# Performance work log

Hardware: AMD Instinct MI355X
Metric: run time of the kernel (lower is better)

The kernel has to match this reference:

```python
import jax, jax.numpy as jnp
import numpy as np

N_NODES = 100000
NUM_GRAPHS = 128
NEG_SLOPE = 0.2


def gat_layer(x, ei, W, a_src, a_dst, b, heads, ch, concat):
    """PyG-style GATConv (v1) with self-loops already included in ei.
    ei[0]=source j, ei[1]=target i; softmax over incoming edges of each target."""
    N = x.shape[0]
    h = (x @ W).reshape(N, heads, ch)                      # [N,H,C]
    asrc = jnp.sum(h * a_src, axis=-1)                     # [N,H]
    adst = jnp.sum(h * a_dst, axis=-1)                     # [N,H]
    src, dst = ei[0], ei[1]
    e = jax.nn.leaky_relu(asrc[src] + adst[dst], NEG_SLOPE)  # [E,H]
    m = jax.ops.segment_max(e, dst, num_segments=N)        # stable softmax per target
    ex = jnp.exp(e - m[dst])
    denom = jax.ops.segment_sum(ex, dst, num_segments=N)
    alpha = ex / denom[dst]                                # [E,H]
    msg = h[src] * alpha[:, :, None]                       # [E,H,C] gather+weight
    out = jax.ops.segment_sum(msg, dst, num_segments=N)    # scatter-add aggregate
    out = out.reshape(N, heads * ch) if concat else out.mean(axis=1)
    return out + b


def setup_inputs() -> dict:
    key = jax.random.key(0)
    ks = jax.random.split(key, 16)
    d_in = 128
    x = jax.random.normal(ks[0], (N_NODES, d_in), dtype=jnp.float32)
    edge_index = jax.random.randint(ks[1], (2, 1600000), 0, N_NODES, dtype=jnp.int64)
    batch = jnp.sort(jax.random.randint(ks[2], (N_NODES,), 0, NUM_GRAPHS, dtype=jnp.int64))
    s = lambda k, shp, fan: jax.random.normal(k, shp, dtype=jnp.float32) / np.sqrt(fan)
    params = dict(
        W1=s(ks[3], (d_in, 4 * 48), d_in),
        a_src1=0.1 * jax.random.normal(ks[4], (4, 48), dtype=jnp.float32),
        a_dst1=0.1 * jax.random.normal(ks[5], (4, 48), dtype=jnp.float32),
        b1=jnp.zeros((4 * 48,), dtype=jnp.float32),
        W2=s(ks[6], (192, 96), 192),
        a_src2=0.1 * jax.random.normal(ks[7], (1, 96), dtype=jnp.float32),
        a_dst2=0.1 * jax.random.normal(ks[8], (1, 96), dtype=jnp.float32),
        b2=jnp.zeros((96,), dtype=jnp.float32),
        fc1_w=s(ks[9], (96, 192), 96),
        fc1_b=jnp.zeros((192,), dtype=jnp.float32),
        fc2_w=s(ks[10], (192, 96), 192),
        fc2_b=jnp.zeros((96,), dtype=jnp.float32),
    )
    return dict(x=x, edge_index=edge_index, batch=batch, **params)


def reference(x, edge_index, batch, W1, a_src1, a_dst1, b1, W2, a_src2, a_dst2, b2,
              fc1_w, fc1_b, fc2_w, fc2_b):
    N = x.shape[0]
    loops = jnp.arange(N, dtype=edge_index.dtype)
    ei = jnp.concatenate([edge_index, jnp.stack([loops, loops])], axis=1)
    h = jax.nn.relu(gat_layer(x, ei, W1, a_src1, a_dst1, b1, heads=4, ch=48, concat=True))
    h = jax.nn.relu(gat_layer(h, ei, W2, a_src2, a_dst2, b2, heads=1, ch=96, concat=True))
    # global mean pool over graphs
    sums = jax.ops.segment_sum(h, batch, num_segments=NUM_GRAPHS)          # [G,96]
    counts = jax.ops.segment_sum(jnp.ones((N,), h.dtype), batch, num_segments=NUM_GRAPHS)
    pooled = sums / jnp.maximum(counts, 1.0)[:, None]
    z = jax.nn.relu(pooled @ fc1_w + fc1_b)
    return z @ fc2_w + fc2_b
```

## Files before the change

### kernel.cpp

```cpp
#include <hip/hip_runtime.h>


#define LRELU(x) fmaxf((x), 0.2f * (x))

using bf16x8 = __attribute__((ext_vector_type(8))) short;
using f32x16 = __attribute__((ext_vector_type(16))) float;

#define NSB 256

__device__ inline unsigned short f2bf(float f) {
  unsigned u = __builtin_bit_cast(unsigned, f);
  return (unsigned short)((u + 0x7fffu + ((u >> 16) & 1u)) >> 16);
}
__device__ inline float bf2f(unsigned short h) {
  return __builtin_bit_cast(float, (unsigned)h << 16);
}
__device__ inline float bfLO(unsigned v) { return __builtin_bit_cast(float, v << 16); }
__device__ inline float bfHI(unsigned v) { return __builtin_bit_cast(float, v & 0xffff0000u); }
__device__ inline unsigned packbf(float a, float b) {
  return (unsigned)f2bf(a) | ((unsigned)f2bf(b) << 16);
}

__device__ inline void wave_lds_fence() {
  __builtin_amdgcn_wave_barrier();
  __builtin_amdgcn_s_waitcnt(0xc07f);
  __builtin_amdgcn_wave_barrier();
}


__global__ __launch_bounds__(256) void k_hist2(const int* __restrict__ dst, int E, int chunk,
                                               int NBK, int* __restrict__ cntmat) {
  __shared__ int lh[512];
  int b = blockIdx.x, t = threadIdx.x;
  for (int i = t; i < NBK; i += 256) lh[i] = 0;
  __syncthreads();
  int beg = b * chunk, end = min(E, beg + chunk);
  for (int e = beg + t; e < end; e += 256) atomicAdd(&lh[dst[e] >> 8], 1);
  __syncthreads();
  for (int i = t; i < NBK; i += 256) cntmat[i * NSB + b] = lh[i];
}

__global__ __launch_bounds__(256) void k_rowscan(int* __restrict__ cntmat,
                                                 int* __restrict__ bucket_tot) {
  int k = blockIdx.x, t = threadIdx.x;
  __shared__ int sc[256];
  int v = cntmat[k * NSB + t];
  sc[t] = v;
  __syncthreads();
  for (int off = 1; off < 256; off <<= 1) {
    int add = (t >= off) ? sc[t - off] : 0;
    __syncthreads();
    sc[t] += add;
    __syncthreads();
  }
  cntmat[k * NSB + t] = sc[t] - v;
  if (t == 255) bucket_tot[k] = sc[t];
}

__global__ __launch_bounds__(512) void k_bscan(const int* __restrict__ bucket_tot, int NBK,
                                               int* __restrict__ bucket_off,
                                               int* __restrict__ row_off, int N, int E) {
  __shared__ int sc[512];
  int t = threadIdx.x;
  int v = (t < NBK) ? bucket_tot[t] : 0;
  sc[t] = v;
  __syncthreads();
  for (int off = 1; off < 512; off <<= 1) {
    int add = (t >= off) ? sc[t - off] : 0;
    __syncthreads();
    sc[t] += add;
    __syncthreads();
  }
  int excl = sc[t] - v;
  if (t < NBK) {
    bucket_off[t] = excl;
    if (t == NBK - 1) bucket_off[NBK] = excl + v;
  }
  if (t == 0) row_off[N] = E + N;
}

__global__ __launch_bounds__(256) void k_scatter2(const int* __restrict__ src,
                                                  const int* __restrict__ dst, int E, int chunk,
                                                  int NBK, const int* __restrict__ bucket_off,
                                                  const int* __restrict__ cntmat,
                                                  int* __restrict__ pairs) {
  __shared__ int base[512];
  __shared__ int cur[512];
  int b = blockIdx.x, t = threadIdx.x;
  for (int i = t; i < NBK; i += 256) {
    base[i] = bucket_off[i] + cntmat[i * NSB + b];
    cur[i] = 0;
  }
  __syncthreads();
  int beg = b * chunk, end = min(E, beg + chunk);
  for (int e = beg + t; e < end; e += 256) {
    int s = src[e], d = dst[e];
    int k = d >> 8;
    int loc = atomicAdd(&cur[k], 1);
    pairs[base[k] + loc] = (s << 8) | (d & 255);
  }
}

#define BBUILD_CAP 8448
__global__ __launch_bounds__(256) void k_bbuild(const int* __restrict__ pairs,
                                                const int* __restrict__ bucket_off,
                                                int N, int* __restrict__ row_off,
                                                int* __restrict__ col) {
  int b = blockIdx.x;
  int t = threadIdx.x;
  int base_d = b * 256;
  int nd = N - base_d;
  if (nd > 256) nd = 256;
  int pbeg = bucket_off[b], pend = bucket_off[b + 1];
  int cntb = pend - pbeg;
  int colbase = pbeg + base_d;

  __shared__ int hist[256];
  __shared__ int scn[256];
  __shared__ int cur[256];
  __shared__ int colL[BBUILD_CAP];
  hist[t] = 0;
  __syncthreads();
  for (int p = pbeg + t; p < pend; p += 256) atomicAdd(&hist[pairs[p] & 255], 1);
  __syncthreads();
  int v = (t < nd) ? hist[t] + 1 : 0;
  scn[t] = v;
  __syncthreads();
  for (int off = 1; off < 256; off <<= 1) {
    int add = (t >= off) ? scn[t - off] : 0;
    __syncthreads();
    scn[t] += add;
    __syncthreads();
  }
  int excl = scn[t] - v;
  if (t < nd) row_off[base_d + t] = colbase + excl;
  int total = cntb + nd;
  if (total <= BBUILD_CAP) {
    cur[t] = excl;
    if (t < nd) colL[excl + hist[t]] = base_d + t;
    __syncthreads();
    for (int p = pbeg + t; p < pend; p += 256) {
      int w = pairs[p];
      int lp = atomicAdd(&cur[w & 255], 1);
      colL[lp] = w >> 8;
    }
    __syncthreads();
    for (int i = t; i < total; i += 256) col[colbase + i] = colL[i];
  } else {
    cur[t] = excl;
    if (t < nd) col[colbase + excl + hist[t]] = base_d + t;
    __syncthreads();
    for (int p = pbeg + t; p < pend; p += 256) {
      int w = pairs[p];
      int lp = atomicAdd(&cur[w & 255], 1);
      col[colbase + lp] = w >> 8;
    }
  }
}


__global__ __launch_bounds__(256) void k_convW(const float* __restrict__ W1,
                                               const float* __restrict__ W2,
                                               unsigned short* __restrict__ T1h,
                                               unsigned short* __restrict__ T1l,
                                               unsigned short* __restrict__ T2h,
                                               unsigned short* __restrict__ T2l) {
  const int E1 = 128 * 192;
  const int E2 = 192 * 96;
  int idx = blockIdx.x * 256 + threadIdx.x;
  if (idx < E1) {
    int k = idx / 192, n = idx - k * 192;
    float w = W1[idx];
    unsigned short hi = f2bf(w);
    unsigned short lo = f2bf(w - bf2f(hi));
    T1h[n * 128 + k] = hi;
    T1l[n * 128 + k] = lo;
  } else if (idx < E1 + E2) {
    int i2 = idx - E1;
    int k = i2 / 96, n = i2 - k * 96;
    float w = W2[i2];
    unsigned short hi = f2bf(w);
    unsigned short lo = f2bf(w - bf2f(hi));
    T2h[n * 192 + k] = hi;
    T2l[n * 192 + k] = lo;
  }
}


template <int K, int N, bool A_BF16>
__global__ __launch_bounds__(256) void k_gemm_mfma(const void* __restrict__ Ap,
                                                   const unsigned short* __restrict__ Bh,
                                                   const unsigned short* __restrict__ Bl,
                                                   unsigned short* __restrict__ C, int M) {
  constexpr int NT = N / 32;
  __shared__ unsigned short As[128 * 40];
  __shared__ unsigned short Bhs[N * 40];
  __shared__ unsigned short Bls[N * 40];
  int tid = threadIdx.x;
  int wave = tid >> 6, lane = tid & 63;
  int bm = blockIdx.x * 128;

  f32x16 acc[NT];
#pragma unroll
  for (int t = 0; t < NT; ++t)
#pragma unroll
    for (int i = 0; i < 16; ++i) acc[t][i] = 0.f;

  for (int k0 = 0; k0 < K; k0 += 32) {
#pragma unroll
    for (int i = 0; i < 2; ++i) {
      int unit = tid + i * 256;
      int r = unit >> 2, u = unit & 3;
      int gr = bm + r;
      uint4 o = make_uint4(0, 0, 0, 0);
      if (gr < M) {
        if (A_BF16) {
          o = *(const uint4*)((const unsigned short*)Ap + (size_t)gr * K + k0 + u * 8);
        } else {
          const float* af = (const float*)Ap + (size_t)gr * K + k0 + u * 8;
          float4 v0 = *(const float4*)af;
          float4 v1 = *(const float4*)(af + 4);
          o.x = (unsigned)f2bf(v0.x) | ((unsigned)f2bf(v0.y) << 16);
          o.y = (unsigned)f2bf(v0.z) | ((unsigned)f2bf(v0.w) << 16);
          o.z = (unsigned)f2bf(v1.x) | ((unsigned)f2bf(v1.y) << 16);
          o.w = (unsigned)f2bf(v1.z) | ((unsigned)f2bf(v1.w) << 16);
        }
      }
      *(uint4*)&As[r * 40 + u * 8] = o;
    }
    for (int unit = tid; unit < N * 4; unit += 256) {
      int n = unit >> 2, u = unit & 3;
      *(uint4*)&Bhs[n * 40 + u * 8] = *(const uint4*)&Bh[n * K + k0 + u * 8];
      *(uint4*)&Bls[n * 40 + u * 8] = *(const uint4*)&Bl[n * K + k0 + u * 8];
    }
    __syncthreads();

    int arow = wave * 32 + (lane & 31);
    int fo = (lane >> 5) * 8;
#pragma unroll
    for (int s = 0; s < 2; ++s) {
      bf16x8 af = *(const bf16x8*)&As[arow * 40 + s * 16 + fo];
#pragma unroll
      for (int t = 0; t < NT; ++t) {
        bf16x8 bh = *(const bf16x8*)&Bhs[(t * 32 + (lane & 31)) * 40 + s * 16 + fo];
        bf16x8 bl = *(const bf16x8*)&Bls[(t * 32 + (lane & 31)) * 40 + s * 16 + fo];
        acc[t] = __builtin_amdgcn_mfma_f32_32x32x16_bf16(af, bh, acc[t], 0, 0, 0);
        acc[t] = __builtin_amdgcn_mfma_f32_32x32x16_bf16(af, bl, acc[t], 0, 0, 0);
      }
    }
    __syncthreads();
  }

#pragma unroll
  for (int t = 0; t < NT; ++t) {
    int col = t * 32 + (lane & 31);
#pragma unroll
    for (int r = 0; r < 16; ++r) {
      int row = wave * 32 + (r & 3) + 8 * (r >> 2) + 4 * (lane >> 5);
      int gr = bm + row;
      if (gr < M) C[(size_t)gr * N + col] = f2bf(acc[t][r]);
    }
  }
}


__global__ __launch_bounds__(256) void k_coef1(const unsigned short* __restrict__ h,
                                               const float* __restrict__ a_src,
                                               const float* __restrict__ a_dst,
                                               float* __restrict__ asrc,
                                               float* __restrict__ adst, int N) {
  int node = blockIdx.x * 4 + (threadIdx.x >> 6);
  if (node >= N) return;
  int m = threadIdx.x & 63;
  const unsigned* hp = (const unsigned*)h + (size_t)node * 96;
  unsigned va = hp[m];
  float x0 = bfLO(va), x1 = bfHI(va);
  float2 as = *(const float2*)&a_src[2 * m];
  float2 ad = *(const float2*)&a_dst[2 * m];
  float pas = x0 * as.x + x1 * as.y;
  float pad = x0 * ad.x + x1 * ad.y;
  int ha = m / 24;
  float pbs = 0.f, pbd = 0.f;
  int hb = (m < 8) ? 2 : 3;
  if (m < 32) {
    unsigned vb = hp[64 + m];
    float y0 = bfLO(vb), y1 = bfHI(vb);
    float2 bs = *(const float2*)&a_src[128 + 2 * m];
    float2 bd = *(const float2*)&a_dst[128 + 2 * m];
    pbs = y0 * bs.x + y1 * bs.y;
    pbd = y0 * bd.x + y1 * bd.y;
  }
  float4 cs, cd;
  cs.x = (ha == 0) ? pas : 0.f;
  cs.y = (ha == 1) ? pas : 0.f;
  cs.z = ((ha == 2) ? pas : 0.f) + ((hb == 2) ? pbs : 0.f);
  cs.w = (hb == 3) ? pbs : 0.f;
  cd.x = (ha == 0) ? pad : 0.f;
  cd.y = (ha == 1) ? pad : 0.f;
  cd.z = ((ha == 2) ? pad : 0.f) + ((hb == 2) ? pbd : 0.f);
  cd.w = (hb == 3) ? pbd : 0.f;
#pragma unroll
  for (int off = 1; off < 64; off <<= 1) {
    cs.x += __shfl_xor(cs.x, off);
    cs.y += __shfl_xor(cs.y, off);
    cs.z += __shfl_xor(cs.z, off);
    cs.w += __shfl_xor(cs.w, off);
    cd.x += __shfl_xor(cd.x, off);
    cd.y += __shfl_xor(cd.y, off);
    cd.z += __shfl_xor(cd.z, off);
    cd.w += __shfl_xor(cd.w, off);
  }
  if (m == 0) {
    *(float4*)&asrc[node * 4] = cs;
    *(float4*)&adst[node * 4] = cd;
  }
}

__global__ __launch_bounds__(256) void k_coef2(const unsigned short* __restrict__ h,
                                               const float* __restrict__ a_src,
                                               const float* __restrict__ a_dst,
                                               float* __restrict__ asrc,
                                               float* __restrict__ adst, int N) {
  int node = blockIdx.x * 4 + (threadIdx.x >> 6);
  if (node >= N) return;
  int m = threadIdx.x & 63;
  float ps = 0.f, pd = 0.f;
  if (m < 48) {
    unsigned v = ((const unsigned*)h)[(size_t)node * 48 + m];
    float x0 = bfLO(v), x1 = bfHI(v);
    float2 as = *(const float2*)&a_src[2 * m];
    float2 ad = *(const float2*)&a_dst[2 * m];
    ps = x0 * as.x + x1 * as.y;
    pd = x0 * ad.x + x1 * ad.y;
  }
#pragma unroll
  for (int off = 1; off < 64; off <<= 1) {
    ps += __shfl_xor(ps, off);
    pd += __shfl_xor(pd, off);
  }
  if (m == 0) {
    asrc[node] = ps;
    adst[node] = pd;
  }
}


__global__ __launch_bounds__(256) void k_agg1(const unsigned short* __restrict__ h,
                                              const float* __restrict__ asrc,
                                              const float* __restrict__ adst,
                                              const int* __restrict__ row_off,
                                              const int* __restrict__ col,
                                              const float* __restrict__ b1,
                                              unsigned short* __restrict__ out, int N) {
  __shared__ int sL[4][64];
  __shared__ float wL[4][64][4];
  int wid = threadIdx.x >> 6;
  int node = blockIdx.x * 4 + wid;
  if (node >= N) return;
  int lane = threadIdx.x & 63;
  int q = lane >> 4;
  int m = lane & 15;
  int hA = m / 6;
  int hB = (m < 4) ? 2 : 3;
  int beg = __builtin_amdgcn_readfirstlane(row_off[node]);
  int end = __builtin_amdgcn_readfirstlane(row_off[node + 1]);
  float4 ad = *(const float4*)&adst[node * 4];
  float accA0 = 0, accA1 = 0, accA2 = 0, accA3 = 0;
  float accA4 = 0, accA5 = 0, accA6 = 0, accA7 = 0;
  float accB0 = 0, accB1 = 0, accB2 = 0, accB3 = 0;
  float da = 0.f, db = 0.f;
  const unsigned* h32 = (const unsigned*)h;
  for (int base = beg; base < end; base += 64) {
    int cnt = end - base;
    if (cnt > 64) cnt = 64;
    int s = 0;
    float w0 = 0.f, w1 = 0.f, w2 = 0.f, w3 = 0.f;
    if (lane < cnt) {
      s = col[base + lane];
      float4 as = *(const float4*)&asrc[s * 4];
      w0 = __expf(LRELU(as.x + ad.x));
      w1 = __expf(LRELU(as.y + ad.y));
      w2 = __expf(LRELU(as.z + ad.z));
      w3 = __expf(LRELU(as.w + ad.w));
    }
    sL[wid][lane] = s;
    *(float4*)&wL[wid][lane][0] = make_float4(w0, w1, w2, w3);
    wave_lds_fence();
    int jmax = (cnt + 3) & ~3;
#pragma unroll 4
    for (int j = 0; j < jmax; j += 4) {
      int je = j + q;
      int sj = sL[wid][je];
      float wa = wL[wid][je][hA];
      float wb = wL[wid][je][hB];
      const unsigned* hp = h32 + (size_t)sj * 96;
      uint4 va = *(const uint4*)(hp + 4 * m);
      uint2 vb = *(const uint2*)(hp + 64 + 2 * m);
      da += wa;
      db += wb;
      accA0 += wa * bfLO(va.x);
      accA1 += wa * bfHI(va.x);
      accA2 += wa * bfLO(va.y);
      accA3 += wa * bfHI(va.y);
      accA4 += wa * bfLO(va.z);
      accA5 += wa * bfHI(va.z);
      accA6 += wa * bfLO(va.w);
      accA7 += wa * bfHI(va.w);
      accB0 += wb * bfLO(vb.x);
      accB1 += wb * bfHI(vb.x);
      accB2 += wb * bfLO(vb.y);
      accB3 += wb * bfHI(vb.y);
    }
    __builtin_amdgcn_wave_barrier();
  }
#define RED2(x) x += __shfl_xor(x, 16); x += __shfl_xor(x, 32)
  RED2(da); RED2(db);
  RED2(accA0); RED2(accA1); RED2(accA2); RED2(accA3);
  RED2(accA4); RED2(accA5); RED2(accA6); RED2(accA7);
  RED2(accB0); RED2(accB1); RED2(accB2); RED2(accB3);
#undef RED2
  if (q == 0) {
    float ra = 1.f / da, rb = 1.f / db;
    float4 biA0 = *(const float4*)&b1[8 * m];
    float4 biA1 = *(const float4*)&b1[8 * m + 4];
    float4 biB = *(const float4*)&b1[128 + 4 * m];
    unsigned* op = (unsigned*)(out + (size_t)node * 192);
    uint4 pa;
    pa.x = packbf(fmaxf(accA0 * ra + biA0.x, 0.f), fmaxf(accA1 * ra + biA0.y, 0.f));
    pa.y = packbf(fmaxf(accA2 * ra + biA0.z, 0.f), fmaxf(accA3 * ra + biA0.w, 0.f));
    pa.z = packbf(fmaxf(accA4 * ra + biA1.x, 0.f), fmaxf(accA5 * ra + biA1.y, 0.f));
    pa.w = packbf(fmaxf(accA6 * ra + biA1.z, 0.f), fmaxf(accA7 * ra + biA1.w, 0.f));
    *(uint4*)(op + 4 * m) = pa;
    uint2 pb;
    pb.x = packbf(fmaxf(accB0 * rb + biB.x, 0.f), fmaxf(accB1 * rb + biB.y, 0.f));
    pb.y = packbf(fmaxf(accB2 * rb + biB.z, 0.f), fmaxf(accB3 * rb + biB.w, 0.f));
    *(uint2*)(op + 64 + 2 * m) = pb;
  }
}

__global__ __launch_bounds__(256) void k_agg2(const unsigned short* __restrict__ h,
                                              const float* __restrict__ asrc,
                                              const float* __restrict__ adst,
                                              const int* __restrict__ row_off,
                                              const int* __restrict__ col,
                                              const float* __restrict__ b2,
                                              float* __restrict__ out, int N) {
  __shared__ int2 eL[4][64];
  int wid = threadIdx.x >> 6;
  int node = blockIdx.x * 4 + wid;
  if (node >= N) return;
  int lane = threadIdx.x & 63;
  int g = lane >> 4;
  int m = lane & 15;
  int beg = __builtin_amdgcn_readfirstlane(row_off[node]);
  int end = __builtin_amdgcn_readfirstlane(row_off[node + 1]);
  float ad = adst[node];
  float a0 = 0, a1 = 0, a2 = 0, a3 = 0, a4 = 0, a5 = 0;
  float den = 0.f;
  const unsigned* h32 = (const unsigned*)h;
  for (int base = beg; base < end; base += 64) {
    int cnt = end - base;
    if (cnt > 64) cnt = 64;
    int s = 0;
    float w = 0.f;
    if (lane < cnt) {
      s = col[base + lane];
      w = __expf(LRELU(asrc[s] + ad));
    }
    eL[wid][lane] = make_int2(s, __builtin_bit_cast(int, w));
    wave_lds_fence();
    int jmax = (cnt + 3) & ~3;
#pragma unroll 4
    for (int j = 0; j < jmax; j += 4) {
      int2 e = eL[wid][j + g];
      int sj = e.x;
      float wj = __builtin_bit_cast(float, e.y);
      den += wj;
      const unsigned* hp = h32 + (size_t)sj * 48;
      uint2 v0 = *(const uint2*)(hp + 2 * m);
      unsigned v1 = hp[32 + m];
      a0 += wj * bfLO(v0.x);
      a1 += wj * bfHI(v0.x);
      a2 += wj * bfLO(v0.y);
      a3 += wj * bfHI(v0.y);
      a4 += wj * bfLO(v1);
      a5 += wj * bfHI(v1);
    }
    __builtin_amdgcn_wave_barrier();
  }
#define RED2(x) x += __shfl_xor(x, 16); x += __shfl_xor(x, 32)
  RED2(den);
  RED2(a0); RED2(a1); RED2(a2); RED2(a3); RED2(a4); RED2(a5);
#undef RED2
  if (g == 0) {
    float r = 1.f / den;
    float* op = out + (size_t)node * 96;
    float4 bi0 = *(const float4*)&b2[4 * m];
    float2 bi1 = *(const float2*)&b2[64 + 2 * m];
    float4 o0;
    o0.x = fmaxf(a0 * r + bi0.x, 0.f);
    o0.y = fmaxf(a1 * r + bi0.y, 0.f);
    o0.z = fmaxf(a2 * r + bi0.z, 0.f);
    o0.w = fmaxf(a3 * r + bi0.w, 0.f);
    *(float4*)(op + 4 * m) = o0;
    float2 o1;
    o1.x = fmaxf(a4 * r + bi1.x, 0.f);
    o1.y = fmaxf(a5 * r + bi1.y, 0.f);
    *(float2*)(op + 64 + 2 * m) = o1;
  }
}


__global__ __launch_bounds__(384) void k_pool_mlp(const float* __restrict__ o2,
                                                  const int* __restrict__ batch, int N,
                                                  const float* __restrict__ fc1w,
                                                  const float* __restrict__ fc1b,
                                                  const float* __restrict__ fc2w,
                                                  const float* __restrict__ fc2b,
                                                  float* __restrict__ out) {
  int g = blockIdx.x;
  int t = threadIdx.x;
  int lo = 0, hi = N;
  while (lo < hi) { int mid = (lo + hi) >> 1; if (batch[mid] < g) lo = mid + 1; else hi = mid; }
  int lo2 = lo;
  int l = lo, hh = N;
  while (l < hh) { int mid = (l + hh) >> 1; if (batch[mid] < g + 1) l = mid + 1; else hh = mid; }
  int hi2 = l;

  __shared__ float part[4][96];
  __shared__ float pooled[96];
  __shared__ float z[192];
  int grp = t / 96, c = t % 96;
  float s = 0.f;
  for (int n = lo2 + grp; n < hi2; n += 4) s += o2[(size_t)n * 96 + c];
  part[grp][c] = s;
  __syncthreads();
  if (t < 96) {
    float tot = part[0][t] + part[1][t] + part[2][t] + part[3][t];
    pooled[t] = tot / fmaxf((float)(hi2 - lo2), 1.0f);
  }
  __syncthreads();
  if (t < 192) {
    float a = fc1b[t];
#pragma unroll 4
    for (int cc = 0; cc < 96; ++cc) a += pooled[cc] * fc1w[cc * 192 + t];
    z[t] = fmaxf(a, 0.f);
  }
  __syncthreads();
  if (t < 96) {
    float a = fc2b[t];
#pragma unroll 4
    for (int j = 0; j < 192; ++j) a += z[j] * fc2w[j * 96 + t];
    out[g * 96 + t] = a;
  }
}


extern "C" void kernel_launch(void* const* d_in, const int* in_sizes, int n_in,
                              void* d_out, int out_size, void* d_ws, size_t ws_size,
                              hipStream_t stream) {
  const float* x = (const float*)d_in[0];
  const int* ei = (const int*)d_in[1];
  const int* batch = (const int*)d_in[2];
  const float* W1 = (const float*)d_in[3];
  const float* a_src1 = (const float*)d_in[4];
  const float* a_dst1 = (const float*)d_in[5];
  const float* b1 = (const float*)d_in[6];
  const float* W2 = (const float*)d_in[7];
  const float* a_src2 = (const float*)d_in[8];
  const float* a_dst2 = (const float*)d_in[9];
  const float* b2 = (const float*)d_in[10];
  const float* fc1w = (const float*)d_in[11];
  const float* fc1b = (const float*)d_in[12];
  const float* fc2w = (const float*)d_in[13];
  const float* fc2b = (const float*)d_in[14];
  float* out = (float*)d_out;

  const int N = in_sizes[2];
  const int E = in_sizes[1] / 2;
  const int G = out_size / 96;
  const int NBK = (N + 255) >> 8;
  const int chunk = (E + NSB - 1) / NSB;

  size_t off = 0;
  auto alloc = [&](size_t bytes) {
    void* p = (char*)d_ws + off;
    off += (bytes + 255) & ~(size_t)255;
    return p;
  };
  unsigned short* h_bf = (unsigned short*)alloc((size_t)N * 192 * 2);
  unsigned short* o1_bf = (unsigned short*)alloc((size_t)N * 192 * 2);
  float* o2_f = (float*)alloc((size_t)N * 96 * 4);
  float* asrc1 = (float*)alloc((size_t)N * 4 * 4);
  float* adst1 = (float*)alloc((size_t)N * 4 * 4);
  float* asrc2 = (float*)alloc((size_t)N * 4);
  float* adst2 = (float*)alloc((size_t)N * 4);
  unsigned short* W1h = (unsigned short*)alloc((size_t)192 * 128 * 2);
  unsigned short* W1l = (unsigned short*)alloc((size_t)192 * 128 * 2);
  unsigned short* W2h = (unsigned short*)alloc((size_t)96 * 192 * 2);
  unsigned short* W2l = (unsigned short*)alloc((size_t)96 * 192 * 2);
  int* row_off = (int*)alloc((size_t)(N + 1) * 4);
  int* col = (int*)alloc((size_t)(E + N) * 4);
  int* pairs = (int*)alloc((size_t)E * 4);
  int* cntmat = (int*)alloc((size_t)NBK * NSB * 4);
  int* bucket_tot = (int*)alloc((size_t)NBK * 4);
  int* bucket_off = (int*)alloc((size_t)(NBK + 1) * 4);
  (void)ws_size;

  const int* src = ei;
  const int* dst = ei + E;

  k_convW<<<(128 * 192 + 192 * 96 + 255) / 256, 256, 0, stream>>>(W1, W2, W1h, W1l, W2h, W2l);

  k_hist2<<<NSB, 256, 0, stream>>>(dst, E, chunk, NBK, cntmat);
  k_rowscan<<<NBK, 256, 0, stream>>>(cntmat, bucket_tot);
  k_bscan<<<1, 512, 0, stream>>>(bucket_tot, NBK, bucket_off, row_off, N, E);
  k_scatter2<<<NSB, 256, 0, stream>>>(src, dst, E, chunk, NBK, bucket_off, cntmat, pairs);
  k_bbuild<<<NBK, 256, 0, stream>>>(pairs, bucket_off, N, row_off, col);

  int gblk = (N + 127) / 128;
  int nblk4 = (N + 3) / 4;

  k_gemm_mfma<128, 192, false><<<gblk, 256, 0, stream>>>(x, W1h, W1l, h_bf, N);
  k_coef1<<<nblk4, 256, 0, stream>>>(h_bf, a_src1, a_dst1, asrc1, adst1, N);
  k_agg1<<<nblk4, 256, 0, stream>>>(h_bf, asrc1, adst1, row_off, col, b1, o1_bf, N);

  k_gemm_mfma<192, 96, true><<<gblk, 256, 0, stream>>>(o1_bf, W2h, W2l, h_bf, N);
  k_coef2<<<nblk4, 256, 0, stream>>>(h_bf, a_src2, a_dst2, asrc2, adst2, N);
  k_agg2<<<nblk4, 256, 0, stream>>>(h_bf, asrc2, adst2, row_off, col, b2, o2_f, N);

  k_pool_mlp<<<G, 384, 0, stream>>>(o2_f, batch, N, fc1w, fc1b, fc2w, fc2b, out);
}
```

Baseline: 518.4 us.

## Split graph pooling across more blocks and lower agg1 inner unroll

```diff
diff --git a/kernel.cpp b/kernel.cpp
--- a/kernel.cpp
+++ b/kernel.cpp
@@ -387,7 +387,7 @@
     *(float4*)&wL[wid][lane][0] = make_float4(w0, w1, w2, w3);
     wave_lds_fence();
     int jmax = (cnt + 3) & ~3;
-#pragma unroll 4
+#pragma unroll 2
     for (int j = 0; j < jmax; j += 4) {
       int je = j + q;
       int sj = sL[wid][je];
@@ -511,13 +511,34 @@
 }
 
 
-__global__ __launch_bounds__(384) void k_pool_mlp(const float* __restrict__ o2,
-                                                  const int* __restrict__ batch, int N,
-                                                  const float* __restrict__ fc1w,
-                                                  const float* __restrict__ fc1b,
-                                                  const float* __restrict__ fc2w,
-                                                  const float* __restrict__ fc2b,
-                                                  float* __restrict__ out) {
+__global__ __launch_bounds__(384) void k_pool(const float* __restrict__ o2,
+                                              const int* __restrict__ batch, int N,
+                                              float* __restrict__ part) {
+  int g = blockIdx.x >> 3;
+  int i = blockIdx.x & 7;
+  int t = threadIdx.x;
+  int grp = t / 96, c = t % 96;
+  int lo = 0, hi = N;
+  while (lo < hi) { int mid = (lo + hi) >> 1; if (batch[mid] < g) lo = mid + 1; else hi = mid; }
+  int lo2 = lo;
+  int l = lo, hh = N;
+  while (l < hh) { int mid = (l + hh) >> 1; if (batch[mid] < g + 1) l = mid + 1; else hh = mid; }
+  int hi2 = l;
+  float s = 0.f;
+  for (int n = lo2 + i + 8 * grp; n < hi2; n += 32) s += o2[(size_t)n * 96 + c];
+  __shared__ float red[4][96];
+  red[grp][c] = s;
+  __syncthreads();
+  if (t < 96) part[(size_t)blockIdx.x * 96 + t] = red[0][t] + red[1][t] + red[2][t] + red[3][t];
+}
+
+__global__ __launch_bounds__(192) void k_mlp(const float* __restrict__ part,
+                                             const int* __restrict__ batch, int N,
+                                             const float* __restrict__ fc1w,
+                                             const float* __restrict__ fc1b,
+                                             const float* __restrict__ fc2w,
+                                             const float* __restrict__ fc2b,
+                                             float* __restrict__ out) {
   int g = blockIdx.x;
   int t = threadIdx.x;
   int lo = 0, hi = N;
@@ -527,20 +548,16 @@
   while (l < hh) { int mid = (l + hh) >> 1; if (batch[mid] < g + 1) l = mid + 1; else hh = mid; }
   int hi2 = l;
 
-  __shared__ float part[4][96];
   __shared__ float pooled[96];
   __shared__ float z[192];
-  int grp = t / 96, c = t % 96;
-  float s = 0.f;
-  for (int n = lo2 + grp; n < hi2; n += 4) s += o2[(size_t)n * 96 + c];
-  part[grp][c] = s;
-  __syncthreads();
   if (t < 96) {
-    float tot = part[0][t] + part[1][t] + part[2][t] + part[3][t];
-    pooled[t] = tot / fmaxf((float)(hi2 - lo2), 1.0f);
-  }
-  __syncthreads();
-  if (t < 192) {
+    float s = 0.f;
+#pragma unroll
+    for (int i = 0; i < 8; ++i) s += part[(size_t)(g * 8 + i) * 96 + t];
+    pooled[t] = s / fmaxf((float)(hi2 - lo2), 1.0f);
+  }
+  __syncthreads();
+  {
     float a = fc1b[t];
 #pragma unroll 4
     for (int cc = 0; cc < 96; ++cc) a += pooled[cc] * fc1w[cc * 192 + t];
@@ -605,6 +622,7 @@
   int* cntmat = (int*)alloc((size_t)NBK * NSB * 4);
   int* bucket_tot = (int*)alloc((size_t)NBK * 4);
   int* bucket_off = (int*)alloc((size_t)(NBK + 1) * 4);
+  float* part = (float*)alloc((size_t)G * 8 * 96 * 4);
   (void)ws_size;
 
   const int* src = ei;
@@ -629,5 +647,6 @@
   k_coef2<<<nblk4, 256, 0, stream>>>(h_bf, a_src2, a_dst2, asrc2, adst2, N);
   k_agg2<<<nblk4, 256, 0, stream>>>(h_bf, asrc2, adst2, row_off, col, b2, o2_f, N);
 
-  k_pool_mlp<<<G, 384, 0, stream>>>(o2_f, batch, N, fc1w, fc1b, fc2w, fc2b, out);
-}
+  k_pool<<<G * 8, 384, 0, stream>>>(o2_f, batch, N, part);
+  k_mlp<<<G, 192, 0, stream>>>(part, batch, N, fc1w, fc1b, fc2w, fc2b, out);
+}
```

Measured after the change: 492.3 us. 1.05x faster.
